# Kernel optimization log

Measured on AMD Instinct MI355X. Metric: run time of the kernel, lower is better.

The kernel has to match this reference:

```python
import jax, jax.numpy as jnp
import numpy as np

GAMMA1, GAMMA2, GAMMA3 = 4.0, 5.0, 10.0
BSIZE = 5
EPS = 1e-10


def _l2norm(x, axis):
    # torch F.normalize: x / max(||x||2, 1e-12)
    n = jnp.sqrt(jnp.sum(x * x, axis=axis, keepdims=True))
    return x / jnp.maximum(n, 1e-12)


def _block_score(v, e, M, HW):
    """calculate_matching_score for one block with uniform segment length.
    v: [B, R, D] flattened image regions (R = M*HW); e: [B, L, D] per-sample texts.
    Segments of the concatenated text are the B chunks of length L (lenAry cumulative).
    """
    B, R, D = v.shape
    L = e.shape[1]
    Tb = B * L
    ef = e.reshape(Tb, D)
    vf = v.reshape(B * R, D)
    s = vf @ ef.T                                        # [B*R, Tb]
    # per-text-segment softmax over text dim, then scale by gamma1
    s_nt = GAMMA1 * jax.nn.softmax(s.reshape(B * R, B, L), axis=-1)
    # attention over image regions
    alpha = jax.nn.softmax(s_nt.reshape(B, R, Tb), axis=1)
    v_tidal = jnp.einsum('brt,brd->btd', alpha, v)       # [B, Tb, D]
    logit = jnp.sum(_l2norm(v_tidal, 2) * _l2norm(ef, 1)[None], axis=2)  # [B, Tb]
    score1 = jnp.sum(jnp.exp(logit).reshape(B, B, L), axis=2)            # [B, B]
    lsm1 = jnp.log(score1 ** (1.0 / GAMMA2) + EPS)
    # beta path: softmax over all regions, exp, reduce over spatial cells
    s_nt2 = jax.nn.softmax(s.reshape(B, R, Tb), axis=1).reshape(B, M, HW, Tb)
    s_exp = jnp.exp(s_nt2)
    sd = jnp.sum(s_exp, axis=2)                          # [B, M, Tb]
    sd4 = sd.reshape(B, M, B, L)
    sd_seg = jnp.sum(sd4, axis=3, keepdims=True)         # per-segment denominators
    beta = sd4 / sd_seg                                  # [B, M, B, L] (= sum_hw s_exp / sd_rep)
    em = jnp.einsum('bmsl,sld->bmsd', beta, e)           # [B, M, B, D] (em_prime)
    # em is constant over the HW repeat axis, so the mean of dot products collapses:
    v_norm_sum = jnp.sum(_l2norm(v.reshape(B, M, HW, D), 3), axis=2)     # [B, M, D]
    logit2 = jnp.einsum('bmsd,bmd->bms', _l2norm(em, 3), v_norm_sum) / HW  # [B, M, B]
    score2 = jnp.sum(jnp.exp(logit2), axis=1) ** (1.0 / GAMMA2)          # [B, B]
    lsm2 = jnp.log(score2 + EPS)
    # beta decorrelation regularizer
    beta_f = beta.reshape(B, M, Tb)
    tmp = jnp.einsum('bmt,bnt->bmn', beta_f, beta_f)     # [B, M, M]
    off = tmp * (1.0 - jnp.eye(M, dtype=tmp.dtype))
    loss_reg = jnp.mean(jnp.sqrt(jnp.sum(off * off, axis=(1, 2))))
    lsm = GAMMA3 * (lsm1 + lsm2)
    d = jnp.diagonal(lsm)
    pdq = -jnp.sum(jnp.log(d / jnp.sum(lsm, axis=1) + EPS))
    pqd = -jnp.sum(jnp.log(d / jnp.sum(lsm, axis=0) + EPS))
    return (pdq + pqd) / B + loss_reg


def setup_inputs() -> dict:
    key = jax.random.key(0)
    k1, k2 = jax.random.split(key)
    B, M, D, H_r, H_w, L = 40, 8, 256, 16, 16, 15
    image = jax.random.normal(k1, (B, M, D, H_r, H_w), dtype=jnp.float32)
    text = jax.random.normal(k2, (B, L, D), dtype=jnp.float32)
    length_info = jnp.full((B,), L, dtype=jnp.int32)  # uniform lengths (max = 15)
    return {'image': image, 'text': text, 'length_info': length_info}


def reference(image, text, length_info):
    B, M, D, H_r, H_w = image.shape
    HW = H_r * H_w
    R = M * HW
    # (shuffle omitted for determinism; identity permutation)
    img = jnp.transpose(image, (0, 1, 3, 4, 2)).reshape(B, R, D)
    nblk = B // BSIZE
    v_blocks = img.reshape(nblk, BSIZE, R, D)
    e_blocks = text.reshape(nblk, BSIZE, text.shape[1], D)
    scores = jax.vmap(lambda v, e: _block_score(v, e, M, HW))(v_blocks, e_blocks)
    numBlcks = B // BSIZE + 1  # faithful to int(B/bsize)+1 in the source
    return jnp.sum(scores) / numBlcks
```

## Files before the change

### kernel.cpp

```cpp
#include <hip/hip_runtime.h>
#include <hip/hip_bf16.h>
#include <math.h>

#define NG 8
#define NB5 5
#define NM 8
#define NHW 256
#define NR 2048
#define ND 256
#define NL 15
#define NT 75
#define NGB 40

#define OFF_S    0
#define SZ_S     (NGB*NT*NR)
#define OFF_W    (OFF_S + SZ_S)
#define OFF_RMAX (OFF_W + SZ_S)
#define SZ_RST   (NGB*5*NR)
#define OFF_RSUM (OFF_RMAX + SZ_RST)
#define OFF_SD   (OFF_RSUM + SZ_RST)
#define SZ_SD    (NGB*NM*NT)
#define OFF_VNS  (OFF_SD + SZ_SD)
#define SZ_VNS   (NGB*NM*ND)
#define OFF_LG   (OFF_VNS + SZ_VNS)
#define SZ_LG    (NGB*NT)
#define OFF_LG2  (OFF_LG + SZ_LG)
#define SZ_LG2   (NGB*NM*5)
#define OFF_BETA (OFF_LG2 + SZ_LG2)
#define SZ_BETA  (NGB*NM*NT)
#define OFF_BLK  (OFF_BETA + SZ_BETA)

#define SHFL_TAIL_ADD(V)                                                       \
    V += __shfl_down(V, 32); V += __shfl_down(V, 16); V += __shfl_down(V, 8);  \
    V += __shfl_down(V, 4);  V += __shfl_down(V, 2);  V += __shfl_down(V, 1);
#define SHFL_TAIL_MAX(V)                                                       \
    V = fmaxf(V, __shfl_down(V, 32)); V = fmaxf(V, __shfl_down(V, 16));        \
    V = fmaxf(V, __shfl_down(V, 8));  V = fmaxf(V, __shfl_down(V, 4));         \
    V = fmaxf(V, __shfl_down(V, 2));  V = fmaxf(V, __shfl_down(V, 1));

__global__ __launch_bounds__(256, 2) void k1_gemm_s(const float* __restrict__ image,
                                                    const float* __restrict__ text,
                                                    float* __restrict__ ws) {
    __shared__ __align__(16) float A[32][260];
    __shared__ __align__(16) float Et[32][52];
    float* Sg = ws + OFF_S;
    int blk = blockIdx.x;
    int th = blk >= 320 ? 1 : 0;
    int rest = blk - th * 320;
    int m = rest & 7, gb = rest >> 3;
    int g = gb / 5;
    int tb = th * 40;
    const float* cell = image + (size_t)(gb * 8 + m) * ND * NHW;
    int tid = threadIdx.x;
    int lane = tid & 63;
    int w = __builtin_amdgcn_readfirstlane(tid >> 6);
    int hw4 = lane * 4;
    int arow = tid >> 6;
    int acol = (tid & 63) * 4;
    int edd  = tid & 31;
    int etc0 = tid >> 5;
    float4 acc[10];
#pragma unroll
    for (int j = 0; j < 10; ++j) acc[j] = make_float4(0.f, 0.f, 0.f, 0.f);
    float4 nsqa = make_float4(0.f, 0.f, 0.f, 0.f);
    float4 p0, p1, p2, p3, p4, p5, p6, p7;
    float e0, e1, e2, e3, e4;
    const float* tbase = text + (size_t)g * 75 * 256;
#define K1_T(I) ((tb + etc0 + 8 * (I)) > 74 ? 74 : (tb + etc0 + 8 * (I)))
#define K1_LOAD(D0)                                                              \
    p0 = *(const float4*)&cell[(size_t)((D0) + arow +  0) * 256 + acol];         \
    p1 = *(const float4*)&cell[(size_t)((D0) + arow +  4) * 256 + acol];         \
    p2 = *(const float4*)&cell[(size_t)((D0) + arow +  8) * 256 + acol];         \
    p3 = *(const float4*)&cell[(size_t)((D0) + arow + 12) * 256 + acol];         \
    p4 = *(const float4*)&cell[(size_t)((D0) + arow + 16) * 256 + acol];         \
    p5 = *(const float4*)&cell[(size_t)((D0) + arow + 20) * 256 + acol];         \
    p6 = *(const float4*)&cell[(size_t)((D0) + arow + 24) * 256 + acol];         \
    p7 = *(const float4*)&cell[(size_t)((D0) + arow + 28) * 256 + acol];         \
    e0 = tbase[(size_t)K1_T(0) * 256 + (D0) + edd];                              \
    e1 = tbase[(size_t)K1_T(1) * 256 + (D0) + edd];                              \
    e2 = tbase[(size_t)K1_T(2) * 256 + (D0) + edd];                              \
    e3 = tbase[(size_t)K1_T(3) * 256 + (D0) + edd];                              \
    e4 = tbase[(size_t)K1_T(4) * 256 + (D0) + edd];
#define K1_ECOL(I) (((etc0 + 8 * (I)) / 10) * 12 + ((etc0 + 8 * (I)) % 10))
    K1_LOAD(0)
    for (int c = 0; c < 8; ++c) {
        __syncthreads();
        *(float4*)&A[arow +  0][acol] = p0;
        *(float4*)&A[arow +  4][acol] = p1;
        *(float4*)&A[arow +  8][acol] = p2;
        *(float4*)&A[arow + 12][acol] = p3;
        *(float4*)&A[arow + 16][acol] = p4;
        *(float4*)&A[arow + 20][acol] = p5;
        *(float4*)&A[arow + 24][acol] = p6;
        *(float4*)&A[arow + 28][acol] = p7;
        Et[edd][K1_ECOL(0)] = e0;
        Et[edd][K1_ECOL(1)] = e1;
        Et[edd][K1_ECOL(2)] = e2;
        Et[edd][K1_ECOL(3)] = e3;
        Et[edd][K1_ECOL(4)] = e4;
        __syncthreads();
        if (c < 7) { K1_LOAD((c + 1) * 32) }
        for (int dd = 0; dd < 32; ++dd) {
            float4 av = *(const float4*)&A[dd][hw4];
            nsqa.x += av.x * av.x; nsqa.y += av.y * av.y;
            nsqa.z += av.z * av.z; nsqa.w += av.w * av.w;
            float4 q0 = *(const float4*)&Et[dd][w * 12];
            float4 q1 = *(const float4*)&Et[dd][w * 12 + 4];
            float2 q2 = *(const float2*)&Et[dd][w * 12 + 8];
            float ev[10] = {q0.x, q0.y, q0.z, q0.w, q1.x, q1.y, q1.z, q1.w, q2.x, q2.y};
#pragma unroll
            for (int j = 0; j < 10; ++j) {
                acc[j].x += av.x * ev[j]; acc[j].y += av.y * ev[j];
                acc[j].z += av.z * ev[j]; acc[j].w += av.w * ev[j];
            }
        }
    }
#undef K1_LOAD
#undef K1_T
#undef K1_ECOL
#pragma unroll
    for (int j = 0; j < 10; ++j) {
        int t = tb + w * 10 + j;
        if (t < 75)
            *(float4*)&Sg[((size_t)gb * 75 + t) * 2048 + m * 256 + hw4] = acc[j];
    }
    if (th == 0 && w == 0)
        *(float4*)&ws[OFF_VNS + (size_t)(gb * 8 + m) * 256 + hw4] = nsqa;
}

__global__ __launch_bounds__(256) void k2_rowstats(float* __restrict__ ws) {
    const float* Sg = ws + OFF_S;
    float* RMAX = ws + OFF_RMAX;
    float* RSUM = ws + OFF_RSUM;
    int blk = blockIdx.x;
    int chunk = blk & 7;
    int rest = blk >> 3;
    int seg = rest % 5, gb = rest / 5;
    int r = chunk * 256 + threadIdx.x;
    const float* base = Sg + (size_t)gb * 75 * 2048 + r;
    float v[15]; float mx = -1e30f;
#pragma unroll
    for (int l = 0; l < 15; ++l) {
        v[l] = base[(size_t)(seg * 15 + l) * 2048];
        mx = fmaxf(mx, v[l]);
    }
    float sm = 0.f;
#pragma unroll
    for (int l = 0; l < 15; ++l) sm += __expf(v[l] - mx);
    RMAX[((size_t)gb * 5 + seg) * 2048 + r] = mx;
    RSUM[((size_t)gb * 5 + seg) * 2048 + r] = sm;
}

__global__ __launch_bounds__(256) void k3_colstats(float* __restrict__ ws) {
    __shared__ float redA[256];
    __shared__ float redB[256];
    __shared__ float red8[8][256];
    __shared__ float bc[2];
    const float* Sg = ws + OFF_S;
    const float* RMAX = ws + OFF_RMAX;
    const float* RSUM = ws + OFF_RSUM;
    float* W = ws + OFF_W;
    float* SD = ws + OFF_SD;
    int blk = blockIdx.x;
    int t = blk % 75, gb = blk / 75;
    int seg = t / 15;
    int tid = threadIdx.x;
    const float* col = Sg + ((size_t)gb * 75 + t) * 2048;
    const float* rmx = RMAX + ((size_t)gb * 5 + seg) * 2048;
    const float* rsm = RSUM + ((size_t)gb * 5 + seg) * 2048;
    float sv[8], ent[8];
    float lmax = -1e30f, lsnt = 0.f;
#pragma unroll
    for (int k = 0; k < 8; ++k) {
        int r = tid + 256 * k;
        float s = col[r];
        sv[k] = s;
        float snt = 4.f * __expf(s - rmx[r]) / rsm[r];
        float e = __expf(snt);
        ent[k] = e;
        lsnt += e;
        lmax = fmaxf(lmax, s);
    }
    redA[tid] = lmax; __syncthreads();
    if (tid < 128) redA[tid] = fmaxf(redA[tid], redA[tid + 128]);
    __syncthreads();
    if (tid < 64) {
        float v = fmaxf(redA[tid], redA[tid + 64]);
        SHFL_TAIL_MAX(v)
        if (tid == 0) bc[0] = v;
    }
    __syncthreads();
    float cmax = bc[0];
    float pe[8]; float lse = 0.f;
#pragma unroll
    for (int k = 0; k < 8; ++k) { pe[k] = __expf(sv[k] - cmax); lse += pe[k]; }
    redA[tid] = lse; redB[tid] = lsnt; __syncthreads();
    if (tid < 128) { redA[tid] += redA[tid + 128]; redB[tid] += redB[tid + 128]; }
    __syncthreads();
    if (tid < 64) {
        float a = redA[tid] + redA[tid + 64];
        float b = redB[tid] + redB[tid + 64];
        SHFL_TAIL_ADD(a)
        SHFL_TAIL_ADD(b)
        if (tid == 0) { bc[0] = 1.f / b; bc[1] = 1.f / a; }
    }
    __syncthreads();
    float inv = bc[0], icsum = bc[1];
#pragma unroll
    for (int k = 0; k < 8; ++k)
        W[((size_t)gb * 75 + t) * 2048 + tid + 256 * k] = ent[k] * inv;
#pragma unroll
    for (int k = 0; k < 8; ++k) red8[k][tid] = __expf(pe[k] * icsum);
    __syncthreads();
    if (tid < 128) {
#pragma unroll
        for (int k = 0; k < 8; ++k) red8[k][tid] += red8[k][tid + 128];
    }
    __syncthreads();
    if (tid < 64) {
        float v[8];
#pragma unroll
        for (int k = 0; k < 8; ++k) v[k] = red8[k][tid] + red8[k][tid + 64];
#pragma unroll
        for (int k = 0; k < 8; ++k) { SHFL_TAIL_ADD(v[k]) }
        if (tid == 0) {
#pragma unroll
            for (int k = 0; k < 8; ++k)
                SD[((size_t)gb * 8 + k) * 75 + t] = v[k];
        }
    }
}

__global__ __launch_bounds__(256, 2) void k4_vtidal(const float* __restrict__ image,
                                                    float* __restrict__ ws) {
    __shared__ __align__(16) float V[32 * 256];
    __shared__ __align__(16) float WtT[32][52];
    const float* W = ws + OFF_W;
    float* VTP = ws + OFF_S;
    int blk = blockIdx.x;
    int th = blk >= 320 ? 1 : 0;
    int rest = blk - th * 320;
    int m = rest & 7, gb = rest >> 3;
    int tb = th * 40;
    const float* cell = image + (size_t)(gb * 8 + m) * ND * NHW;
    int tid = threadIdx.x;
    int lane = tid & 63;
    int w = __builtin_amdgcn_readfirstlane(tid >> 6);
    int d4 = lane * 4;
    int rr4  = (tid & 7) * 4;
    int drow = tid >> 3;
    int wrr  = tid & 31;
    int wtc0 = tid >> 5;
    float4 acc[10];
#pragma unroll
    for (int j = 0; j < 10; ++j) acc[j] = make_float4(0.f, 0.f, 0.f, 0.f);
    const float* wb = W + (size_t)gb * 75 * 2048 + m * 256;
    float4 p0, p1, p2, p3, p4, p5, p6, p7;
    float w0, w1, w2, w3, w4;
#define K4_T(I) ((tb + wtc0 + 8 * (I)) > 74 ? 74 : (tb + wtc0 + 8 * (I)))
#define K4_LOAD(RC)                                                               \
    p0 = *(const float4*)&cell[(size_t)(drow +   0) * 256 + (RC) * 32 + rr4];     \
    p1 = *(const float4*)&cell[(size_t)(drow +  32) * 256 + (RC) * 32 + rr4];     \
    p2 = *(const float4*)&cell[(size_t)(drow +  64) * 256 + (RC) * 32 + rr4];     \
    p3 = *(const float4*)&cell[(size_t)(drow +  96) * 256 + (RC) * 32 + rr4];     \
    p4 = *(const float4*)&cell[(size_t)(drow + 128) * 256 + (RC) * 32 + rr4];     \
    p5 = *(const float4*)&cell[(size_t)(drow + 160) * 256 + (RC) * 32 + rr4];     \
    p6 = *(const float4*)&cell[(size_t)(drow + 192) * 256 + (RC) * 32 + rr4];     \
    p7 = *(const float4*)&cell[(size_t)(drow + 224) * 256 + (RC) * 32 + rr4];     \
    w0 = wb[(size_t)K4_T(0) * 2048 + (RC) * 32 + wrr];                            \
    w1 = wb[(size_t)K4_T(1) * 2048 + (RC) * 32 + wrr];                            \
    w2 = wb[(size_t)K4_T(2) * 2048 + (RC) * 32 + wrr];                            \
    w3 = wb[(size_t)K4_T(3) * 2048 + (RC) * 32 + wrr];                            \
    w4 = wb[(size_t)K4_T(4) * 2048 + (RC) * 32 + wrr];
#define K4_WCOL(I) (((wtc0 + 8 * (I)) / 10) * 12 + ((wtc0 + 8 * (I)) % 10))
#define K4_VADDR(RR, D) (((RR) << 8) + ((((D) >> 2) ^ (((RR) >> 2) & 7)) << 2) + ((D) & 3))
#define K4_VST(P, DOFF)                                                           \
    V[K4_VADDR(rr4 + 0, drow + (DOFF))] = (P).x;                                  \
    V[K4_VADDR(rr4 + 1, drow + (DOFF))] = (P).y;                                  \
    V[K4_VADDR(rr4 + 2, drow + (DOFF))] = (P).z;                                  \
    V[K4_VADDR(rr4 + 3, drow + (DOFF))] = (P).w;
    K4_LOAD(0)
    for (int rc = 0; rc < 8; ++rc) {
        __syncthreads();
        K4_VST(p0,   0) K4_VST(p1,  32) K4_VST(p2,  64) K4_VST(p3,  96)
        K4_VST(p4, 128) K4_VST(p5, 160) K4_VST(p6, 192) K4_VST(p7, 224)
        WtT[wrr][K4_WCOL(0)] = w0;
        WtT[wrr][K4_WCOL(1)] = w1;
        WtT[wrr][K4_WCOL(2)] = w2;
        WtT[wrr][K4_WCOL(3)] = w3;
        WtT[wrr][K4_WCOL(4)] = w4;
        __syncthreads();
        if (rc < 7) { K4_LOAD(rc + 1) }
        for (int rr = 0; rr < 32; ++rr) {
            int sr = (rr >> 2) & 7;
            float4 vv = *(const float4*)&V[(rr << 8) + ((lane ^ sr) << 2)];
            float4 q0 = *(const float4*)&WtT[rr][w * 12];
            float4 q1 = *(const float4*)&WtT[rr][w * 12 + 4];
            float2 q2 = *(const float2*)&WtT[rr][w * 12 + 8];
            float wv[10] = {q0.x, q0.y, q0.z, q0.w, q1.x, q1.y, q1.z, q1.w, q2.x, q2.y};
#pragma unroll
            for (int j = 0; j < 10; ++j) {
                acc[j].x += vv.x * wv[j]; acc[j].y += vv.y * wv[j];
                acc[j].z += vv.z * wv[j]; acc[j].w += vv.w * wv[j];
            }
        }
    }
#undef K4_LOAD
#undef K4_T
#undef K4_WCOL
#undef K4_VADDR
#undef K4_VST
#pragma unroll
    for (int j = 0; j < 10; ++j) {
        int t = tb + w * 10 + j;
        if (t < 75)
            *(float4*)&VTP[((size_t)(gb * 8 + m) * 75 + t) * 256 + d4] = acc[j];
    }
}

__global__ __launch_bounds__(256) void k5_logit(const float* __restrict__ text,
                                                float* __restrict__ ws) {
    __shared__ float rA[256], rB[256], rC[256];
    const float* VTP = ws + OFF_S;
    float* LG = ws + OFF_LG;
    int blk = blockIdx.x;
    int t = blk % 75, gb = blk / 75, g = gb / 5;
    int tid = threadIdx.x;
    float vt = 0.f;
#pragma unroll
    for (int m = 0; m < 8; ++m)
        vt += VTP[((size_t)(gb * 8 + m) * 75 + t) * 256 + tid];
    int seg = t / 15, l = t % 15;
    float ev = text[((size_t)(g * 5 + seg) * 15 + l) * 256 + tid];
    rA[tid] = vt * vt; rB[tid] = ev * ev; rC[tid] = vt * ev;
    __syncthreads();
    if (tid < 128) {
        rA[tid] += rA[tid + 128];
        rB[tid] += rB[tid + 128];
        rC[tid] += rC[tid + 128];
    }
    __syncthreads();
    if (tid < 64) {
        float a = rA[tid] + rA[tid + 64];
        float b = rB[tid] + rB[tid + 64];
        float c = rC[tid] + rC[tid + 64];
        SHFL_TAIL_ADD(a)
        SHFL_TAIL_ADD(b)
        SHFL_TAIL_ADD(c)
        if (tid == 0)
            LG[gb * 75 + t] = c / (fmaxf(sqrtf(a), 1e-12f) * fmaxf(sqrtf(b), 1e-12f));
    }
}

__global__ __launch_bounds__(256) void k6_vns(const float* __restrict__ image,
                                              const float* __restrict__ text,
                                              float* __restrict__ ws) {
    __shared__ float A[32][257];
    __shared__ float rn[256];
    __shared__ float ps[256];
    __shared__ float vns_s[256];
    __shared__ float rA[256], rB[256];
    __shared__ float sdv[75];
    __shared__ float segs[5];
    __shared__ float betas[5][15];
    const float* SD = ws + OFF_SD;
    float* BETA = ws + OFF_BETA;
    float* LG2 = ws + OFF_LG2;
    int blk = blockIdx.x;
    int m = blk & 7, gb = blk >> 3, g = gb / 5;
    const float* cell = image + (size_t)(gb * 8 + m) * ND * NHW;
    int tid = threadIdx.x;
    float nsq = ws[OFF_VNS + (size_t)(gb * 8 + m) * 256 + tid];
    rn[tid] = 1.f / fmaxf(sqrtf(nsq), 1e-12f);
    if (tid < 75) sdv[tid] = SD[((size_t)gb * 8 + m) * 75 + tid];
    int d_loc = tid & 31, sub = tid >> 5;
    for (int d0 = 0; d0 < 256; d0 += 32) {
        __syncthreads();
#pragma unroll
        for (int i = 0; i < 32; ++i) A[i][tid] = cell[(d0 + i) * 256 + tid];
        __syncthreads();
        float partial = 0.f;
#pragma unroll
        for (int k = 0; k < 32; ++k) {
            int hw = sub + 8 * k;
            partial += A[d_loc][hw] * rn[hw];
        }
        ps[tid] = partial; __syncthreads();
        if (tid < 128) ps[tid] += ps[tid + 128];
        __syncthreads();
        if (tid < 64) ps[tid] += ps[tid + 64];
        __syncthreads();
        if (tid < 32)
            vns_s[d0 + tid] = ps[tid] + ps[tid + 32];
    }
    __syncthreads();
    if (tid < 5) {
        float s = 0.f;
        for (int l = 0; l < 15; ++l) s += sdv[tid * 15 + l];
        segs[tid] = s;
    }
    __syncthreads();
    if (tid < 75) {
        float b = sdv[tid] / segs[tid / 15];
        betas[tid / 15][tid % 15] = b;
        BETA[((size_t)gb * 8 + m) * 75 + tid] = b;
    }
    __syncthreads();
    float vns = vns_s[tid];
    for (int s = 0; s < 5; ++s) {
        float em = 0.f;
#pragma unroll
        for (int l = 0; l < 15; ++l)
            em += betas[s][l] * text[((size_t)(g * 5 + s) * 15 + l) * 256 + tid];
        rA[tid] = em * em; rB[tid] = em * vns;
        __syncthreads();
        if (tid < 128) { rA[tid] += rA[tid + 128]; rB[tid] += rB[tid + 128]; }
        __syncthreads();
        if (tid < 64) {
            float a = rA[tid] + rA[tid + 64];
            float b = rB[tid] + rB[tid + 64];
            SHFL_TAIL_ADD(a)
            SHFL_TAIL_ADD(b)
            if (tid == 0)
                LG2[((size_t)gb * 8 + m) * 5 + s] =
                    b / fmaxf(sqrtf(a), 1e-12f) * (1.f / 256.f);
        }
        __syncthreads();
    }
}

__global__ __launch_bounds__(256) void k8_final(float* __restrict__ ws) {
    __shared__ float lsm[5][5];
    __shared__ float offsq[5][64];
    __shared__ float regs[5];
    const float* LG = ws + OFF_LG;
    const float* LG2 = ws + OFF_LG2;
    const float* BETA = ws + OFF_BETA;
    float* BLK = ws + OFF_BLK;
    int g = blockIdx.x;
    int tid = threadIdx.x;
    if (tid < 25) {
        int b = tid / 5, s = tid % 5;
        int gb = g * 5 + b;
        float s1 = 0.f;
        for (int l = 0; l < 15; ++l) s1 += expf(LG[gb * 75 + s * 15 + l]);
        float s2 = 0.f;
        for (int mm = 0; mm < 8; ++mm) s2 += expf(LG2[((size_t)gb * 8 + mm) * 5 + s]);
        float l1 = logf(powf(s1, 0.2f) + 1e-10f);
        float l2 = logf(powf(s2, 0.2f) + 1e-10f);
        lsm[b][s] = 10.f * (l1 + l2);
    }
    for (int p = tid; p < 320; p += 256) {
        int b = p >> 6, mn = p & 63, mm = mn >> 3, nn = mn & 7;
        int gb = g * 5 + b;
        const float* bm = BETA + ((size_t)gb * 8 + mm) * 75;
        const float* bn = BETA + ((size_t)gb * 8 + nn) * 75;
        float acc = 0.f;
        for (int t2 = 0; t2 < 75; ++t2) acc += bm[t2] * bn[t2];
        offsq[b][mn] = (mm == nn) ? 0.f : acc * acc;
    }
    __syncthreads();
    if (tid < 5) {
        float s = 0.f;
        for (int i = 0; i < 64; ++i) s += offsq[tid][i];
        regs[tid] = sqrtf(s);
    }
    __syncthreads();
    if (tid == 0) {
        float loss_reg = 0.f;
        for (int b = 0; b < 5; ++b) loss_reg += regs[b];
        loss_reg *= 0.2f;
        float pdq = 0.f, pqd = 0.f;
        for (int i = 0; i < 5; ++i) {
            float rsum = 0.f, csum = 0.f;
            for (int j = 0; j < 5; ++j) { rsum += lsm[i][j]; csum += lsm[j][i]; }
            float di = lsm[i][i];
            pdq += -logf(di / rsum + 1e-10f);
            pqd += -logf(di / csum + 1e-10f);
        }
        BLK[g] = (pdq + pqd) * 0.2f + loss_reg;
    }
}

__global__ void k9_out(const float* __restrict__ ws, float* __restrict__ out) {
    if (threadIdx.x == 0) {
        float s = 0.f;
        for (int g2 = 0; g2 < 8; ++g2) s += ws[OFF_BLK + g2];
        out[0] = s / 9.f;
    }
}

extern "C" void kernel_launch(void* const* d_in, const int* in_sizes, int n_in,
                              void* d_out, int out_size, void* d_ws, size_t ws_size,
                              hipStream_t stream) {
    const float* image = (const float*)d_in[0];
    const float* text  = (const float*)d_in[1];
    float* ws = (float*)d_ws;
    float* out = (float*)d_out;
    hipLaunchKernelGGL(k1_gemm_s,   dim3(640),  dim3(256), 0, stream, image, text, ws);
    hipLaunchKernelGGL(k2_rowstats, dim3(1600), dim3(256), 0, stream, ws);
    hipLaunchKernelGGL(k3_colstats, dim3(3000), dim3(256), 0, stream, ws);
    hipLaunchKernelGGL(k4_vtidal,   dim3(640),  dim3(256), 0, stream, image, ws);
    hipLaunchKernelGGL(k5_logit,    dim3(3000), dim3(256), 0, stream, text, ws);
    hipLaunchKernelGGL(k6_vns,      dim3(320),  dim3(256), 0, stream, image, text, ws);
    hipLaunchKernelGGL(k8_final,    dim3(8),    dim3(256), 0, stream, ws);
    hipLaunchKernelGGL(k9_out,      dim3(1),    dim3(64),  0, stream, ws, out);
}
```

Baseline: 272.9 us.

## Retile score GEMM to split spatial dim into quarters with all texts per block

The first GEMM kernel now tiles over a quarter of the spatial cells (64) per block and computes all 75 text columns, instead of all 256 cells with half the texts. This doubles the grid to 1280 blocks and cuts the image staging per block. Each thread now holds 19 scalar accumulators instead of 10 float4s. The intent is better occupancy and less redundant image reads. The cost is more text reads per block, scalar rather than float4 stores, and more LDS traffic per FMA.

```diff
diff --git a/kernel.cpp b/kernel.cpp
--- a/kernel.cpp
+++ b/kernel.cpp
@@ -41,91 +41,93 @@
 __global__ __launch_bounds__(256, 2) void k1_gemm_s(const float* __restrict__ image,
                                                     const float* __restrict__ text,
                                                     float* __restrict__ ws) {
-    __shared__ __align__(16) float A[32][260];
-    __shared__ __align__(16) float Et[32][52];
+    __shared__ __align__(16) float A[32][68];
+    __shared__ __align__(16) float Et[32][80];
     float* Sg = ws + OFF_S;
     int blk = blockIdx.x;
-    int th = blk >= 320 ? 1 : 0;
-    int rest = blk - th * 320;
+    int hq = blk / 320;
+    int rest = blk - hq * 320;
     int m = rest & 7, gb = rest >> 3;
     int g = gb / 5;
-    int tb = th * 40;
+    int hwbase = hq * 64;
     const float* cell = image + (size_t)(gb * 8 + m) * ND * NHW;
+    const float* tbase = text + (size_t)g * 75 * 256;
     int tid = threadIdx.x;
     int lane = tid & 63;
     int w = __builtin_amdgcn_readfirstlane(tid >> 6);
-    int hw4 = lane * 4;
-    int arow = tid >> 6;
-    int acol = (tid & 63) * 4;
+    int srow = tid >> 4;
+    int scol = (tid & 15) * 4;
     int edd  = tid & 31;
     int etc0 = tid >> 5;
-    float4 acc[10];
-#pragma unroll
-    for (int j = 0; j < 10; ++j) acc[j] = make_float4(0.f, 0.f, 0.f, 0.f);
-    float4 nsqa = make_float4(0.f, 0.f, 0.f, 0.f);
-    float4 p0, p1, p2, p3, p4, p5, p6, p7;
-    float e0, e1, e2, e3, e4;
-    const float* tbase = text + (size_t)g * 75 * 256;
-#define K1_T(I) ((tb + etc0 + 8 * (I)) > 74 ? 74 : (tb + etc0 + 8 * (I)))
+    int te[10], ec[10];
+#pragma unroll
+    for (int i = 0; i < 10; ++i) {
+        int t = etc0 + 8 * i;
+        int tc = t > 74 ? 74 : t;
+        te[i] = tc;
+        ec[i] = (tc / 19) * 20 + (tc % 19);
+    }
+    float acc[19];
+#pragma unroll
+    for (int j = 0; j < 19; ++j) acc[j] = 0.f;
+    float nsqa = 0.f;
+    float4 p0, p1;
+    float e0, e1, e2, e3, e4, e5, e6, e7, e8, e9;
 #define K1_LOAD(D0)                                                              \
-    p0 = *(const float4*)&cell[(size_t)((D0) + arow +  0) * 256 + acol];         \
-    p1 = *(const float4*)&cell[(size_t)((D0) + arow +  4) * 256 + acol];         \
-    p2 = *(const float4*)&cell[(size_t)((D0) + arow +  8) * 256 + acol];         \
-    p3 = *(const float4*)&cell[(size_t)((D0) + arow + 12) * 256 + acol];         \
-    p4 = *(const float4*)&cell[(size_t)((D0) + arow + 16) * 256 + acol];         \
-    p5 = *(const float4*)&cell[(size_t)((D0) + arow + 20) * 256 + acol];         \
-    p6 = *(const float4*)&cell[(size_t)((D0) + arow + 24) * 256 + acol];         \
-    p7 = *(const float4*)&cell[(size_t)((D0) + arow + 28) * 256 + acol];         \
-    e0 = tbase[(size_t)K1_T(0) * 256 + (D0) + edd];                              \
-    e1 = tbase[(size_t)K1_T(1) * 256 + (D0) + edd];                              \
-    e2 = tbase[(size_t)K1_T(2) * 256 + (D0) + edd];                              \
-    e3 = tbase[(size_t)K1_T(3) * 256 + (D0) + edd];                              \
-    e4 = tbase[(size_t)K1_T(4) * 256 + (D0) + edd];
-#define K1_ECOL(I) (((etc0 + 8 * (I)) / 10) * 12 + ((etc0 + 8 * (I)) % 10))
+    p0 = *(const float4*)&cell[(size_t)((D0) + srow) * 256 + hwbase + scol];     \
+    p1 = *(const float4*)&cell[(size_t)((D0) + srow + 16) * 256 + hwbase + scol];\
+    e0 = tbase[(size_t)te[0] * 256 + (D0) + edd];                                \
+    e1 = tbase[(size_t)te[1] * 256 + (D0) + edd];                                \
+    e2 = tbase[(size_t)te[2] * 256 + (D0) + edd];                                \
+    e3 = tbase[(size_t)te[3] * 256 + (D0) + edd];                                \
+    e4 = tbase[(size_t)te[4] * 256 + (D0) + edd];                                \
+    e5 = tbase[(size_t)te[5] * 256 + (D0) + edd];                                \
+    e6 = tbase[(size_t)te[6] * 256 + (D0) + edd];                                \
+    e7 = tbase[(size_t)te[7] * 256 + (D0) + edd];                                \
+    e8 = tbase[(size_t)te[8] * 256 + (D0) + edd];                                \
+    e9 = tbase[(size_t)te[9] * 256 + (D0) + edd];
     K1_LOAD(0)
     for (int c = 0; c < 8; ++c) {
         __syncthreads();
-        *(float4*)&A[arow +  0][acol] = p0;
-        *(float4*)&A[arow +  4][acol] = p1;
-        *(float4*)&A[arow +  8][acol] = p2;
-        *(float4*)&A[arow + 12][acol] = p3;
-        *(float4*)&A[arow + 16][acol] = p4;
-        *(float4*)&A[arow + 20][acol] = p5;
-        *(float4*)&A[arow + 24][acol] = p6;
-        *(float4*)&A[arow + 28][acol] = p7;
-        Et[edd][K1_ECOL(0)] = e0;
-        Et[edd][K1_ECOL(1)] = e1;
-        Et[edd][K1_ECOL(2)] = e2;
-        Et[edd][K1_ECOL(3)] = e3;
-        Et[edd][K1_ECOL(4)] = e4;
+        *(float4*)&A[srow][scol] = p0;
+        *(float4*)&A[srow + 16][scol] = p1;
+        Et[edd][ec[0]] = e0;
+        Et[edd][ec[1]] = e1;
+        Et[edd][ec[2]] = e2;
+        Et[edd][ec[3]] = e3;
+        Et[edd][ec[4]] = e4;
+        Et[edd][ec[5]] = e5;
+        Et[edd][ec[6]] = e6;
+        Et[edd][ec[7]] = e7;
+        Et[edd][ec[8]] = e8;
+        Et[edd][ec[9]] = e9;
         __syncthreads();
         if (c < 7) { K1_LOAD((c + 1) * 32) }
         for (int dd = 0; dd < 32; ++dd) {
-            float4 av = *(const float4*)&A[dd][hw4];
-            nsqa.x += av.x * av.x; nsqa.y += av.y * av.y;
-            nsqa.z += av.z * av.z; nsqa.w += av.w * av.w;
-            float4 q0 = *(const float4*)&Et[dd][w * 12];
-            float4 q1 = *(const float4*)&Et[dd][w * 12 + 4];
-            float2 q2 = *(const float2*)&Et[dd][w * 12 + 8];
-            float ev[10] = {q0.x, q0.y, q0.z, q0.w, q1.x, q1.y, q1.z, q1.w, q2.x, q2.y};
-#pragma unroll
-            for (int j = 0; j < 10; ++j) {
-                acc[j].x += av.x * ev[j]; acc[j].y += av.y * ev[j];
-                acc[j].z += av.z * ev[j]; acc[j].w += av.w * ev[j];
-            }
+            float a = A[dd][lane];
+            nsqa += a * a;
+            float4 q0 = *(const float4*)&Et[dd][w * 20];
+            float4 q1 = *(const float4*)&Et[dd][w * 20 + 4];
+            float4 q2 = *(const float4*)&Et[dd][w * 20 + 8];
+            float4 q3 = *(const float4*)&Et[dd][w * 20 + 12];
+            float4 q4 = *(const float4*)&Et[dd][w * 20 + 16];
+            float ev[19] = {q0.x, q0.y, q0.z, q0.w, q1.x, q1.y, q1.z, q1.w,
+                            q2.x, q2.y, q2.z, q2.w, q3.x, q3.y, q3.z, q3.w,
+                            q4.x, q4.y, q4.z};
+#pragma unroll
+            for (int j = 0; j < 19; ++j) acc[j] += a * ev[j];
         }
     }
 #undef K1_LOAD
-#undef K1_T
-#undef K1_ECOL
-#pragma unroll
-    for (int j = 0; j < 10; ++j) {
-        int t = tb + w * 10 + j;
+    int t0 = w * 19;
+#pragma unroll
+    for (int j = 0; j < 19; ++j) {
+        int t = t0 + j;
         if (t < 75)
-            *(float4*)&Sg[((size_t)gb * 75 + t) * 2048 + m * 256 + hw4] = acc[j];
-    }
-    if (th == 0 && w == 0)
-        *(float4*)&ws[OFF_VNS + (size_t)(gb * 8 + m) * 256 + hw4] = nsqa;
+            Sg[((size_t)gb * 75 + t) * 2048 + m * 256 + hwbase + lane] = acc[j];
+    }
+    if (w == 0)
+        ws[OFF_VNS + (size_t)(gb * 8 + m) * 256 + hwbase + lane] = nsqa;
 }
 
 __global__ __launch_bounds__(256) void k2_rowstats(float* __restrict__ ws) {
@@ -497,7 +499,7 @@
     const float* text  = (const float*)d_in[1];
     float* ws = (float*)d_ws;
     float* out = (float*)d_out;
-    hipLaunchKernelGGL(k1_gemm_s,   dim3(640),  dim3(256), 0, stream, image, text, ws);
+    hipLaunchKernelGGL(k1_gemm_s,   dim3(1280), dim3(256), 0, stream, image, text, ws);
     hipLaunchKernelGGL(k2_rowstats, dim3(1600), dim3(256), 0, stream, ws);
     hipLaunchKernelGGL(k3_colstats, dim3(3000), dim3(256), 0, stream, ws);
     hipLaunchKernelGGL(k4_vtidal,   dim3(640),  dim3(256), 0, stream, image, ws);
```

Result: slower. 299.7 us (+9.8%).
